# Kernel optimization log

Hardware: AMD Instinct MI355X
Metric: run time of the kernel (lower is better)

## Reference

```python
import jax, jax.numpy as jnp
import numpy as np

BS, DIM = 8192, 768
TEMPERATURE = 1.0
EPS = 1e-8


def setup_inputs() -> dict:
    key = jax.random.key(0)
    k1, k2 = jax.random.split(key)
    text_emb = jax.random.normal(k1, (BS, DIM), dtype=jnp.float32)
    ctr_emb = jax.random.normal(k2, (BS, DIM), dtype=jnp.float32)
    return {"text_emb": text_emb, "ctr_emb": ctr_emb}


def _l2norm(x):
    # cosine scorer normalization
    return x / jnp.maximum(jnp.linalg.norm(x, axis=-1, keepdims=True), EPS)


def reference(text_emb, ctr_emb):
    t = _l2norm(text_emb)          # [bs, d]
    c = _l2norm(ctr_emb)           # [bs, d]
    # S[i, j] = cos(text_i, ctr_j) / T  -- single GEMM instead of (bs,bs,d) broadcast
    S = jnp.einsum('id,jd->ij', t, c) / TEMPERATURE   # [bs, bs]
    sim_ii = jnp.diagonal(S)                           # [bs]
    # loss1_i = lse_j S[i,j] - S[i,i]; loss2_i = lse_j S[j,i] - S[i,i]
    loss = (jax.nn.logsumexp(S, axis=1)
            + jax.nn.logsumexp(S, axis=0)
            - 2.0 * sim_ii)
    return jnp.mean(loss)
```

## Files before the change

kernel.cpp:

```cpp
#include <hip/hip_runtime.h>
#include <hip/hip_bf16.h>

#define BS   8192
#define DIM  768
#define BM   256
#define BK   128
#define NBLK ((BS / BM) * (BS / BM))

typedef float f32x4 __attribute__((ext_vector_type(4)));
typedef int   i32x4 __attribute__((ext_vector_type(4)));
typedef int   i32x8 __attribute__((ext_vector_type(8)));

__device__ __forceinline__ void async16(const void* g, void* l) {
    __builtin_amdgcn_global_load_lds(
        (const __attribute__((address_space(1))) unsigned int*)g,
        (__attribute__((address_space(3))) unsigned int*)l,
        16, 0, 0);
}

__global__ __launch_bounds__(256) void normalize_kernel(
    const float* __restrict__ text, const float* __restrict__ ctr,
    unsigned char* __restrict__ tq, unsigned char* __restrict__ cq,
    float* __restrict__ sim, float* __restrict__ rowsum, float* __restrict__ colsum,
    unsigned int* __restrict__ cnt) {
    if (blockIdx.x < 64) {
        const int i = blockIdx.x * 256 + threadIdx.x;
        rowsum[i] = 0.f;
        colsum[i] = 0.f;
    }
    if (blockIdx.x == 0 && threadIdx.x == 0) cnt[0] = 0u;
    const int lane = threadIdx.x & 63;
    const int row  = blockIdx.x * 4 + (threadIdx.x >> 6);
    const size_t base = (size_t)row * DIM;

    float4 t[3], c[3];
    float st = 0.f, sc = 0.f, sd = 0.f;
#pragma unroll
    for (int i = 0; i < 3; ++i) {
        t[i] = *(const float4*)&text[base + lane * 4 + i * 256];
        c[i] = *(const float4*)&ctr [base + lane * 4 + i * 256];
        st += t[i].x*t[i].x + t[i].y*t[i].y + t[i].z*t[i].z + t[i].w*t[i].w;
        sc += c[i].x*c[i].x + c[i].y*c[i].y + c[i].z*c[i].z + c[i].w*c[i].w;
        sd += t[i].x*c[i].x + t[i].y*c[i].y + t[i].z*c[i].z + t[i].w*c[i].w;
    }
#pragma unroll
    for (int off = 1; off < 64; off <<= 1) {
        st += __shfl_xor(st, off);
        sc += __shfl_xor(sc, off);
        sd += __shfl_xor(sd, off);
    }
    const float invt = 1.0f / fmaxf(sqrtf(st), 1e-8f);
    const float invc = 1.0f / fmaxf(sqrtf(sc), 1e-8f);
#pragma unroll
    for (int i = 0; i < 3; ++i) {
        unsigned int wt = (unsigned int)__builtin_amdgcn_cvt_pk_fp8_f32(t[i].x * invt, t[i].y * invt, 0, false);
        wt = (unsigned int)__builtin_amdgcn_cvt_pk_fp8_f32(t[i].z * invt, t[i].w * invt, (int)wt, true);
        unsigned int wcq = (unsigned int)__builtin_amdgcn_cvt_pk_fp8_f32(c[i].x * invc, c[i].y * invc, 0, false);
        wcq = (unsigned int)__builtin_amdgcn_cvt_pk_fp8_f32(c[i].z * invc, c[i].w * invc, (int)wcq, true);
        *(unsigned int*)&tq[base + lane * 4 + i * 256] = wt;
        *(unsigned int*)&cq[base + lane * 4 + i * 256] = wcq;
    }
    if (lane == 0) sim[row] = sd * invt * invc;
}

__global__ __launch_bounds__(512, 2) void gemm_lse_kernel(
    const unsigned char* __restrict__ tq, const unsigned char* __restrict__ cq,
    float* __restrict__ rowsum, float* __restrict__ colsum,
    const float* __restrict__ sim, unsigned int* __restrict__ cnt,
    float* __restrict__ out) {
    __shared__ char ldsA[2][BM * BK];
    __shared__ char ldsB[2][BM * BK];

    const int tid = threadIdx.x;

    const int bid = blockIdx.x;
    const int xcd = bid & 7, idx = bid >> 3;
    const int tileCol = idx >> 2, rowInBand = idx & 3;
    const int rowBase = (xcd * 4 + rowInBand) * BM;
    const int colBase = tileCol * BM;

    const int wave = tid >> 6, lane = tid & 63;
    const int wr = wave >> 2, wc = wave & 3;
    const int quad = lane >> 4, l16 = lane & 15;

    int goff[4], p16[4];
#pragma unroll
    for (int i = 0; i < 4; ++i) {
        const int p  = tid + i * 512;
        const int kc = p >> 9;
        const int row = (p >> 1) & 255;
        const int hl  = (p & 1) ^ (kc & 1);
        goff[i] = row * DIM + kc * 32 + hl * 16;
        p16[i]  = p * 16;
    }
    const unsigned char* gA = tq + (size_t)rowBase * DIM;
    const unsigned char* gB = cq + (size_t)colBase * DIM;

#define STAGE(buf, t, i)                                            \
    do {                                                            \
        async16(gA + goff[i] + (t) * BK, &ldsA[buf][p16[i]]);       \
        async16(gB + goff[i] + (t) * BK, &ldsB[buf][p16[i]]);       \
    } while (0)

    const int sw = quad & 1;
    int aoff[8], boff[4];
#pragma unroll
    for (int mt = 0; mt < 8; ++mt) aoff[mt] = quad * 8192 + (wr * 128 + mt * 16 + l16) * 32;
#pragma unroll
    for (int nt = 0; nt < 4; ++nt) boff[nt] = quad * 8192 + (wc * 64 + nt * 16 + l16) * 32;

#define RD_A(dst, mt, buf)                                                     \
    do {                                                                       \
        i32x4 lo = *(const i32x4*)(ldsA[buf] + aoff[mt] + sw * 16);            \
        i32x4 hi = *(const i32x4*)(ldsA[buf] + aoff[mt] + (sw ^ 1) * 16);      \
        dst = __builtin_shufflevector(lo, hi, 0, 1, 2, 3, 4, 5, 6, 7);         \
    } while (0)
#define RD_B(dst, nt, buf)                                                     \
    do {                                                                       \
        i32x4 lo = *(const i32x4*)(ldsB[buf] + boff[nt] + sw * 16);            \
        i32x4 hi = *(const i32x4*)(ldsB[buf] + boff[nt] + (sw ^ 1) * 16);      \
        dst = __builtin_shufflevector(lo, hi, 0, 1, 2, 3, 4, 5, 6, 7);         \
    } while (0)
#define MFMA8(a0, a1, m0, m1)                                                  \
    do {                                                                       \
        acc[m0][0] = __builtin_amdgcn_mfma_scale_f32_16x16x128_f8f6f4(a0, bf0, acc[m0][0], 0, 0, 0, 127, 0, 127); \
        acc[m0][1] = __builtin_amdgcn_mfma_scale_f32_16x16x128_f8f6f4(a0, bf1, acc[m0][1], 0, 0, 0, 127, 0, 127); \
        acc[m0][2] = __builtin_amdgcn_mfma_scale_f32_16x16x128_f8f6f4(a0, bf2, acc[m0][2], 0, 0, 0, 127, 0, 127); \
        acc[m0][3] = __builtin_amdgcn_mfma_scale_f32_16x16x128_f8f6f4(a0, bf3, acc[m0][3], 0, 0, 0, 127, 0, 127); \
        acc[m1][0] = __builtin_amdgcn_mfma_scale_f32_16x16x128_f8f6f4(a1, bf0, acc[m1][0], 0, 0, 0, 127, 0, 127); \
        acc[m1][1] = __builtin_amdgcn_mfma_scale_f32_16x16x128_f8f6f4(a1, bf1, acc[m1][1], 0, 0, 0, 127, 0, 127); \
        acc[m1][2] = __builtin_amdgcn_mfma_scale_f32_16x16x128_f8f6f4(a1, bf2, acc[m1][2], 0, 0, 0, 127, 0, 127); \
        acc[m1][3] = __builtin_amdgcn_mfma_scale_f32_16x16x128_f8f6f4(a1, bf3, acc[m1][3], 0, 0, 0, 127, 0, 127); \
    } while (0)
#define SBAR()  __builtin_amdgcn_sched_barrier(0)

    f32x4 acc[8][4];
#pragma unroll
    for (int mt = 0; mt < 8; ++mt)
#pragma unroll
        for (int nt = 0; nt < 4; ++nt)
            acc[mt][nt] = (f32x4){0.f, 0.f, 0.f, 0.f};

    STAGE(0, 0, 0); STAGE(0, 0, 1); STAGE(0, 0, 2); STAGE(0, 0, 3);
    SBAR();
    STAGE(1, 1, 0);
    SBAR();
    asm volatile("s_waitcnt vmcnt(2)" ::: "memory");
    SBAR();
    __builtin_amdgcn_s_barrier();

#pragma unroll
    for (int t = 0; t < 6; ++t) {
        const int cur = t & 1;
        i32x8 bf0, bf1, bf2, bf3, aE0, aE1, aO0, aO1;

        RD_B(bf0, 0, cur); RD_B(bf1, 1, cur); RD_B(bf2, 2, cur); RD_B(bf3, 3, cur);
        RD_A(aE0, 0, cur); RD_A(aE1, 1, cur);

        RD_A(aO0, 2, cur); RD_A(aO1, 3, cur);
        if (t < 5) STAGE(cur ^ 1, t + 1, 1);
        __builtin_amdgcn_s_barrier();
        asm volatile("s_waitcnt lgkmcnt(4)" ::: "memory");
        SBAR();
        __builtin_amdgcn_s_setprio(1);
        MFMA8(aE0, aE1, 0, 1);
        __builtin_amdgcn_s_setprio(0);
        __builtin_amdgcn_s_barrier();

        RD_A(aE0, 4, cur); RD_A(aE1, 5, cur);
        if (t < 5) STAGE(cur ^ 1, t + 1, 2);
        __builtin_amdgcn_s_barrier();
        asm volatile("s_waitcnt lgkmcnt(4)" ::: "memory");
        SBAR();
        __builtin_amdgcn_s_setprio(1);
        MFMA8(aO0, aO1, 2, 3);
        __builtin_amdgcn_s_setprio(0);
        __builtin_amdgcn_s_barrier();

        RD_A(aO0, 6, cur); RD_A(aO1, 7, cur);
        if (t < 5) STAGE(cur ^ 1, t + 1, 3);
        __builtin_amdgcn_s_barrier();
        asm volatile("s_waitcnt lgkmcnt(4)" ::: "memory");
        SBAR();
        __builtin_amdgcn_s_setprio(1);
        MFMA8(aE0, aE1, 4, 5);
        __builtin_amdgcn_s_setprio(0);
        __builtin_amdgcn_s_barrier();

        asm volatile("s_waitcnt lgkmcnt(0)" ::: "memory");
        SBAR();
        if (t < 5) {
            __builtin_amdgcn_s_barrier();
            if (t < 4) STAGE(cur, t + 2, 0);
        }
        __builtin_amdgcn_s_setprio(1);
        MFMA8(aO0, aO1, 6, 7);
        __builtin_amdgcn_s_setprio(0);
        if (t < 5) {
            if (t < 4) asm volatile("s_waitcnt vmcnt(2)" ::: "memory");
            else       asm volatile("s_waitcnt vmcnt(0)" ::: "memory");
            SBAR();
            __builtin_amdgcn_s_barrier();
        }
    }

    float rp[8][4];
    float cp[4];
#pragma unroll
    for (int mt = 0; mt < 8; ++mt)
#pragma unroll
        for (int r = 0; r < 4; ++r) rp[mt][r] = 0.f;
#pragma unroll
    for (int nt = 0; nt < 4; ++nt) cp[nt] = 0.f;

#pragma unroll
    for (int mt = 0; mt < 8; ++mt)
#pragma unroll
        for (int nt = 0; nt < 4; ++nt)
#pragma unroll
            for (int r = 0; r < 4; ++r) {
                const float e = __expf(acc[mt][nt][r]);
                rp[mt][r] += e;
                cp[nt]    += e;
            }

#pragma unroll
    for (int mt = 0; mt < 8; ++mt)
#pragma unroll
        for (int r = 0; r < 4; ++r) {
            float v = rp[mt][r];
            v += __shfl_xor(v, 1);
            v += __shfl_xor(v, 2);
            v += __shfl_xor(v, 4);
            v += __shfl_xor(v, 8);
            rp[mt][r] = v;
        }
    if (l16 == 0) {
#pragma unroll
        for (int mt = 0; mt < 8; ++mt)
#pragma unroll
            for (int r = 0; r < 4; ++r)
                atomicAdd(&rowsum[rowBase + wr * 128 + mt * 16 + quad * 4 + r], rp[mt][r]);
    }
#pragma unroll
    for (int nt = 0; nt < 4; ++nt) {
        float v = cp[nt];
        v += __shfl_xor(v, 16);
        v += __shfl_xor(v, 32);
        if (quad == 0)
            atomicAdd(&colsum[colBase + wc * 64 + nt * 16 + l16], v);
    }

    unsigned int* tick = (unsigned int*)&ldsA[0][0];
    __syncthreads();
    if (tid == 0) {
        __threadfence();
        tick[0] = __hip_atomic_fetch_add(cnt, 1u, __ATOMIC_ACQ_REL, __HIP_MEMORY_SCOPE_AGENT);
    }
    __syncthreads();
    if (tick[0] == NBLK - 1) {
        float a2 = 0.f;
#pragma unroll
        for (int k = 0; k < 16; ++k) {
            const int i = tid + k * 512;
            const float rs = __hip_atomic_load(&rowsum[i], __ATOMIC_RELAXED, __HIP_MEMORY_SCOPE_AGENT);
            const float cs = __hip_atomic_load(&colsum[i], __ATOMIC_RELAXED, __HIP_MEMORY_SCOPE_AGENT);
            a2 += __logf(rs) + __logf(cs) - 2.f * sim[i];
        }
#pragma unroll
        for (int off = 1; off < 64; off <<= 1) a2 += __shfl_xor(a2, off);
        float* red = (float*)&ldsB[0][0];
        if (lane == 0) red[wave] = a2;
        __syncthreads();
        if (tid == 0) {
            float s = 0.f;
#pragma unroll
            for (int w = 0; w < 8; ++w) s += red[w];
            out[0] = s / (float)BS;
        }
    }
}

extern "C" void kernel_launch(void* const* d_in, const int* in_sizes, int n_in,
                              void* d_out, int out_size, void* d_ws, size_t ws_size,
                              hipStream_t stream) {
    const float* text = (const float*)d_in[0];
    const float* ctr  = (const float*)d_in[1];

    char* ws = (char*)d_ws;
    const size_t embBytes = (size_t)BS * DIM;
    unsigned char* tq = (unsigned char*)ws;
    unsigned char* cq = (unsigned char*)(ws + embBytes);
    float* sim    = (float*)(ws + 2 * embBytes);
    float* rowsum = (float*)(ws + 2 * embBytes + BS * sizeof(float));
    float* colsum = (float*)(ws + 2 * embBytes + 2 * BS * sizeof(float));
    unsigned int* cnt = (unsigned int*)(ws + 2 * embBytes + 3 * BS * sizeof(float));

    normalize_kernel<<<BS / 4, 256, 0, stream>>>(text, ctr, tq, cq, sim, rowsum, colsum, cnt);

    gemm_lse_kernel<<<NBLK, 512, 0, stream>>>(tq, cq, rowsum, colsum, sim, cnt, (float*)d_out);
}
```

Baseline: 200.7 us.

## Fuse normalize and GEMM-LSE into one persistent kernel with grid barrier

Merges the normalize/quantize kernel and the GEMM+logsumexp kernel into a single persistent launch of 256 blocks. The blocks first normalize rows, then meet at a global atomic grid barrier, and each block then processes 4 column tiles in a loop. The extra per-stage s_barriers inside the K loop are also dropped. This removes one kernel launch and the tail of the second grid, but it relies on all 256 blocks being co-resident, adds a memset launch, and gives up some latency hiding from the removed barriers.

```diff
diff --git a/kernel.cpp b/kernel.cpp
--- a/kernel.cpp
+++ b/kernel.cpp
@@ -1,11 +1,11 @@
 #include <hip/hip_runtime.h>
 #include <hip/hip_bf16.h>
 
-#define BS   8192
-#define DIM  768
-#define BM   256
-#define BK   128
-#define NBLK ((BS / BM) * (BS / BM))
+#define BS    8192
+#define DIM   768
+#define BM    256
+#define BK    128
+#define NPERS 256
 
 typedef float f32x4 __attribute__((ext_vector_type(4)));
 typedef int   i32x4 __attribute__((ext_vector_type(4)));
@@ -18,70 +18,72 @@
         16, 0, 0);
 }
 
-__global__ __launch_bounds__(256) void normalize_kernel(
+__global__ __launch_bounds__(512, 2) void fused_kernel(
     const float* __restrict__ text, const float* __restrict__ ctr,
     unsigned char* __restrict__ tq, unsigned char* __restrict__ cq,
     float* __restrict__ sim, float* __restrict__ rowsum, float* __restrict__ colsum,
-    unsigned int* __restrict__ cnt) {
-    if (blockIdx.x < 64) {
-        const int i = blockIdx.x * 256 + threadIdx.x;
+    unsigned int* __restrict__ syncv, float* __restrict__ out) {
+    __shared__ char ldsA[2][BM * BK];
+    __shared__ char ldsB[2][BM * BK];
+
+    const int tid  = threadIdx.x;
+    const int bid  = blockIdx.x;
+    const int wave = tid >> 6, lane = tid & 63;
+
+    if (bid < 32) {
+        const int i = bid * 512 + tid;
         rowsum[i] = 0.f;
         colsum[i] = 0.f;
     }
-    if (blockIdx.x == 0 && threadIdx.x == 0) cnt[0] = 0u;
-    const int lane = threadIdx.x & 63;
-    const int row  = blockIdx.x * 4 + (threadIdx.x >> 6);
-    const size_t base = (size_t)row * DIM;
-
-    float4 t[3], c[3];
-    float st = 0.f, sc = 0.f, sd = 0.f;
-#pragma unroll
-    for (int i = 0; i < 3; ++i) {
-        t[i] = *(const float4*)&text[base + lane * 4 + i * 256];
-        c[i] = *(const float4*)&ctr [base + lane * 4 + i * 256];
-        st += t[i].x*t[i].x + t[i].y*t[i].y + t[i].z*t[i].z + t[i].w*t[i].w;
-        sc += c[i].x*c[i].x + c[i].y*c[i].y + c[i].z*c[i].z + c[i].w*c[i].w;
-        sd += t[i].x*c[i].x + t[i].y*c[i].y + t[i].z*c[i].z + t[i].w*c[i].w;
-    }
-#pragma unroll
-    for (int off = 1; off < 64; off <<= 1) {
-        st += __shfl_xor(st, off);
-        sc += __shfl_xor(sc, off);
-        sd += __shfl_xor(sd, off);
-    }
-    const float invt = 1.0f / fmaxf(sqrtf(st), 1e-8f);
-    const float invc = 1.0f / fmaxf(sqrtf(sc), 1e-8f);
-#pragma unroll
-    for (int i = 0; i < 3; ++i) {
-        unsigned int wt = (unsigned int)__builtin_amdgcn_cvt_pk_fp8_f32(t[i].x * invt, t[i].y * invt, 0, false);
-        wt = (unsigned int)__builtin_amdgcn_cvt_pk_fp8_f32(t[i].z * invt, t[i].w * invt, (int)wt, true);
-        unsigned int wcq = (unsigned int)__builtin_amdgcn_cvt_pk_fp8_f32(c[i].x * invc, c[i].y * invc, 0, false);
-        wcq = (unsigned int)__builtin_amdgcn_cvt_pk_fp8_f32(c[i].z * invc, c[i].w * invc, (int)wcq, true);
-        *(unsigned int*)&tq[base + lane * 4 + i * 256] = wt;
-        *(unsigned int*)&cq[base + lane * 4 + i * 256] = wcq;
-    }
-    if (lane == 0) sim[row] = sd * invt * invc;
-}
-
-__global__ __launch_bounds__(512, 2) void gemm_lse_kernel(
-    const unsigned char* __restrict__ tq, const unsigned char* __restrict__ cq,
-    float* __restrict__ rowsum, float* __restrict__ colsum,
-    const float* __restrict__ sim, unsigned int* __restrict__ cnt,
-    float* __restrict__ out) {
-    __shared__ char ldsA[2][BM * BK];
-    __shared__ char ldsB[2][BM * BK];
-
-    const int tid = threadIdx.x;
-
-    const int bid = blockIdx.x;
-    const int xcd = bid & 7, idx = bid >> 3;
-    const int tileCol = idx >> 2, rowInBand = idx & 3;
-    const int rowBase = (xcd * 4 + rowInBand) * BM;
-    const int colBase = tileCol * BM;
-
-    const int wave = tid >> 6, lane = tid & 63;
+#pragma unroll
+    for (int r = 0; r < 4; ++r) {
+        const int row = bid * 32 + wave * 4 + r;
+        const size_t base = (size_t)row * DIM;
+        float4 t[3], c[3];
+        float st = 0.f, sc = 0.f, sd = 0.f;
+#pragma unroll
+        for (int i = 0; i < 3; ++i) {
+            t[i] = *(const float4*)&text[base + lane * 4 + i * 256];
+            c[i] = *(const float4*)&ctr [base + lane * 4 + i * 256];
+            st += t[i].x*t[i].x + t[i].y*t[i].y + t[i].z*t[i].z + t[i].w*t[i].w;
+            sc += c[i].x*c[i].x + c[i].y*c[i].y + c[i].z*c[i].z + c[i].w*c[i].w;
+            sd += t[i].x*c[i].x + t[i].y*c[i].y + t[i].z*c[i].z + t[i].w*c[i].w;
+        }
+#pragma unroll
+        for (int off = 1; off < 64; off <<= 1) {
+            st += __shfl_xor(st, off);
+            sc += __shfl_xor(sc, off);
+            sd += __shfl_xor(sd, off);
+        }
+        const float invt = 1.0f / fmaxf(sqrtf(st), 1e-8f);
+        const float invc = 1.0f / fmaxf(sqrtf(sc), 1e-8f);
+#pragma unroll
+        for (int i = 0; i < 3; ++i) {
+            unsigned int wt = (unsigned int)__builtin_amdgcn_cvt_pk_fp8_f32(t[i].x * invt, t[i].y * invt, 0, false);
+            wt = (unsigned int)__builtin_amdgcn_cvt_pk_fp8_f32(t[i].z * invt, t[i].w * invt, (int)wt, true);
+            unsigned int wcq = (unsigned int)__builtin_amdgcn_cvt_pk_fp8_f32(c[i].x * invc, c[i].y * invc, 0, false);
+            wcq = (unsigned int)__builtin_amdgcn_cvt_pk_fp8_f32(c[i].z * invc, c[i].w * invc, (int)wcq, true);
+            *(unsigned int*)&tq[base + lane * 4 + i * 256] = wt;
+            *(unsigned int*)&cq[base + lane * 4 + i * 256] = wcq;
+        }
+        if (lane == 0) sim[row] = sd * invt * invc;
+    }
+
+    __syncthreads();
+    if (tid == 0) {
+        __threadfence();
+        __hip_atomic_fetch_add(&syncv[0], 1u, __ATOMIC_ACQ_REL, __HIP_MEMORY_SCOPE_AGENT);
+        while (__hip_atomic_load(&syncv[0], __ATOMIC_RELAXED, __HIP_MEMORY_SCOPE_AGENT) < NPERS)
+            __builtin_amdgcn_s_sleep(1);
+        __threadfence();
+    }
+    __syncthreads();
+
     const int wr = wave >> 2, wc = wave & 3;
     const int quad = lane >> 4, l16 = lane & 15;
+
+    const int rowBase = ((bid & 7) * 4 + ((bid >> 3) & 3)) * BM;
+    const unsigned char* gA = tq + (size_t)rowBase * DIM;
 
     int goff[4], p16[4];
 #pragma unroll
@@ -93,22 +95,19 @@
         goff[i] = row * DIM + kc * 32 + hl * 16;
         p16[i]  = p * 16;
     }
-    const unsigned char* gA = tq + (size_t)rowBase * DIM;
-    const unsigned char* gB = cq + (size_t)colBase * DIM;
+
+    const int sw = quad & 1;
+    int aoff[8], boff[4];
+#pragma unroll
+    for (int mt = 0; mt < 8; ++mt) aoff[mt] = quad * 8192 + (wr * 128 + mt * 16 + l16) * 32;
+#pragma unroll
+    for (int nt = 0; nt < 4; ++nt) boff[nt] = quad * 8192 + (wc * 64 + nt * 16 + l16) * 32;
 
 #define STAGE(buf, t, i)                                            \
     do {                                                            \
         async16(gA + goff[i] + (t) * BK, &ldsA[buf][p16[i]]);       \
         async16(gB + goff[i] + (t) * BK, &ldsB[buf][p16[i]]);       \
     } while (0)
-
-    const int sw = quad & 1;
-    int aoff[8], boff[4];
-#pragma unroll
-    for (int mt = 0; mt < 8; ++mt) aoff[mt] = quad * 8192 + (wr * 128 + mt * 16 + l16) * 32;
-#pragma unroll
-    for (int nt = 0; nt < 4; ++nt) boff[nt] = quad * 8192 + (wc * 64 + nt * 16 + l16) * 32;
-
 #define RD_A(dst, mt, buf)                                                     \
     do {                                                                       \
         i32x4 lo = *(const i32x4*)(ldsA[buf] + aoff[mt] + sw * 16);            \
@@ -134,131 +133,137 @@
     } while (0)
 #define SBAR()  __builtin_amdgcn_sched_barrier(0)
 
-    f32x4 acc[8][4];
-#pragma unroll
-    for (int mt = 0; mt < 8; ++mt)
-#pragma unroll
-        for (int nt = 0; nt < 4; ++nt)
-            acc[mt][nt] = (f32x4){0.f, 0.f, 0.f, 0.f};
-
-    STAGE(0, 0, 0); STAGE(0, 0, 1); STAGE(0, 0, 2); STAGE(0, 0, 3);
-    SBAR();
-    STAGE(1, 1, 0);
-    SBAR();
-    asm volatile("s_waitcnt vmcnt(2)" ::: "memory");
-    SBAR();
-    __builtin_amdgcn_s_barrier();
-
-#pragma unroll
-    for (int t = 0; t < 6; ++t) {
-        const int cur = t & 1;
-        i32x8 bf0, bf1, bf2, bf3, aE0, aE1, aO0, aO1;
-
-        RD_B(bf0, 0, cur); RD_B(bf1, 1, cur); RD_B(bf2, 2, cur); RD_B(bf3, 3, cur);
-        RD_A(aE0, 0, cur); RD_A(aE1, 1, cur);
-
-        RD_A(aO0, 2, cur); RD_A(aO1, 3, cur);
-        if (t < 5) STAGE(cur ^ 1, t + 1, 1);
+#pragma unroll 1
+    for (int rep = 0; rep < 4; ++rep) {
+        const int colBase = (rep * 8 + (bid >> 5)) * BM;
+        const unsigned char* gB = cq + (size_t)colBase * DIM;
+
+        f32x4 acc[8][4];
+#pragma unroll
+        for (int mt = 0; mt < 8; ++mt)
+#pragma unroll
+            for (int nt = 0; nt < 4; ++nt)
+                acc[mt][nt] = (f32x4){0.f, 0.f, 0.f, 0.f};
+
+        __syncthreads();
+
+        STAGE(0, 0, 0); STAGE(0, 0, 1); STAGE(0, 0, 2); STAGE(0, 0, 3);
+        SBAR();
+        STAGE(1, 1, 0);
+        SBAR();
+        asm volatile("s_waitcnt vmcnt(2)" ::: "memory");
+        SBAR();
         __builtin_amdgcn_s_barrier();
-        asm volatile("s_waitcnt lgkmcnt(4)" ::: "memory");
-        SBAR();
-        __builtin_amdgcn_s_setprio(1);
-        MFMA8(aE0, aE1, 0, 1);
-        __builtin_amdgcn_s_setprio(0);
-        __builtin_amdgcn_s_barrier();
-
-        RD_A(aE0, 4, cur); RD_A(aE1, 5, cur);
-        if (t < 5) STAGE(cur ^ 1, t + 1, 2);
-        __builtin_amdgcn_s_barrier();
-        asm volatile("s_waitcnt lgkmcnt(4)" ::: "memory");
-        SBAR();
-        __builtin_amdgcn_s_setprio(1);
-        MFMA8(aO0, aO1, 2, 3);
-        __builtin_amdgcn_s_setprio(0);
-        __builtin_amdgcn_s_barrier();
-
-        RD_A(aO0, 6, cur); RD_A(aO1, 7, cur);
-        if (t < 5) STAGE(cur ^ 1, t + 1, 3);
-        __builtin_amdgcn_s_barrier();
-        asm volatile("s_waitcnt lgkmcnt(4)" ::: "memory");
-        SBAR();
-        __builtin_amdgcn_s_setprio(1);
-        MFMA8(aE0, aE1, 4, 5);
-        __builtin_amdgcn_s_setprio(0);
-        __builtin_amdgcn_s_barrier();
-
-        asm volatile("s_waitcnt lgkmcnt(0)" ::: "memory");
-        SBAR();
-        if (t < 5) {
-            __builtin_amdgcn_s_barrier();
-            if (t < 4) STAGE(cur, t + 2, 0);
-        }
-        __builtin_amdgcn_s_setprio(1);
-        MFMA8(aO0, aO1, 6, 7);
-        __builtin_amdgcn_s_setprio(0);
-        if (t < 5) {
-            if (t < 4) asm volatile("s_waitcnt vmcnt(2)" ::: "memory");
-            else       asm volatile("s_waitcnt vmcnt(0)" ::: "memory");
+
+#pragma unroll
+        for (int t = 0; t < 6; ++t) {
+            const int cur = t & 1;
+            i32x8 bf0, bf1, bf2, bf3, aE0, aE1, aO0, aO1;
+
+            RD_B(bf0, 0, cur); RD_B(bf1, 1, cur); RD_B(bf2, 2, cur); RD_B(bf3, 3, cur);
+            RD_A(aE0, 0, cur); RD_A(aE1, 1, cur);
+
+            RD_A(aO0, 2, cur); RD_A(aO1, 3, cur);
+            if (t < 5) STAGE(cur ^ 1, t + 1, 1);
+            asm volatile("s_waitcnt lgkmcnt(4)" ::: "memory");
             SBAR();
-            __builtin_amdgcn_s_barrier();
-        }
-    }
-
-    float rp[8][4];
-    float cp[4];
-#pragma unroll
-    for (int mt = 0; mt < 8; ++mt)
-#pragma unroll
-        for (int r = 0; r < 4; ++r) rp[mt][r] = 0.f;
-#pragma unroll
-    for (int nt = 0; nt < 4; ++nt) cp[nt] = 0.f;
-
-#pragma unroll
-    for (int mt = 0; mt < 8; ++mt)
-#pragma unroll
-        for (int nt = 0; nt < 4; ++nt)
+            __builtin_amdgcn_s_setprio(1);
+            MFMA8(aE0, aE1, 0, 1);
+            __builtin_amdgcn_s_setprio(0);
+
+            RD_A(aE0, 4, cur); RD_A(aE1, 5, cur);
+            if (t < 5) STAGE(cur ^ 1, t + 1, 2);
+            asm volatile("s_waitcnt lgkmcnt(4)" ::: "memory");
+            SBAR();
+            __builtin_amdgcn_s_setprio(1);
+            MFMA8(aO0, aO1, 2, 3);
+            __builtin_amdgcn_s_setprio(0);
+
+            RD_A(aO0, 6, cur); RD_A(aO1, 7, cur);
+            if (t < 5) STAGE(cur ^ 1, t + 1, 3);
+            asm volatile("s_waitcnt lgkmcnt(4)" ::: "memory");
+            SBAR();
+            __builtin_amdgcn_s_setprio(1);
+            MFMA8(aE0, aE1, 4, 5);
+            __builtin_amdgcn_s_setprio(0);
+
+            asm volatile("s_waitcnt lgkmcnt(0)" ::: "memory");
+            SBAR();
+            __builtin_amdgcn_s_setprio(1);
+            MFMA8(aO0, aO1, 6, 7);
+            __builtin_amdgcn_s_setprio(0);
+
+            if (t < 5) {
+                __builtin_amdgcn_s_barrier();
+                SBAR();
+                if (t < 4) {
+                    STAGE(cur, t + 2, 0);
+                    SBAR();
+                    asm volatile("s_waitcnt vmcnt(2)" ::: "memory");
+                } else {
+                    asm volatile("s_waitcnt vmcnt(0)" ::: "memory");
+                }
+                SBAR();
+                __builtin_amdgcn_s_barrier();
+            }
+        }
+
+        float rp[8][4];
+        float cp[4];
+#pragma unroll
+        for (int mt = 0; mt < 8; ++mt)
+#pragma unroll
+            for (int r = 0; r < 4; ++r) rp[mt][r] = 0.f;
+#pragma unroll
+        for (int nt = 0; nt < 4; ++nt) cp[nt] = 0.f;
+
+#pragma unroll
+        for (int mt = 0; mt < 8; ++mt)
+#pragma unroll
+            for (int nt = 0; nt < 4; ++nt)
+#pragma unroll
+                for (int r = 0; r < 4; ++r) {
+                    const float e = __expf(acc[mt][nt][r]);
+                    rp[mt][r] += e;
+                    cp[nt]    += e;
+                }
+
+#pragma unroll
+        for (int mt = 0; mt < 8; ++mt)
 #pragma unroll
             for (int r = 0; r < 4; ++r) {
-                const float e = __expf(acc[mt][nt][r]);
-                rp[mt][r] += e;
-                cp[nt]    += e;
+                float v = rp[mt][r];
+                v += __shfl_xor(v, 1);
+                v += __shfl_xor(v, 2);
+                v += __shfl_xor(v, 4);
+                v += __shfl_xor(v, 8);
+                rp[mt][r] = v;
             }
-
-#pragma unroll
-    for (int mt = 0; mt < 8; ++mt)
-#pragma unroll
-        for (int r = 0; r < 4; ++r) {
-            float v = rp[mt][r];
-            v += __shfl_xor(v, 1);
-            v += __shfl_xor(v, 2);
-            v += __shfl_xor(v, 4);
-            v += __shfl_xor(v, 8);
-            rp[mt][r] = v;
-        }
-    if (l16 == 0) {
-#pragma unroll
-        for (int mt = 0; mt < 8; ++mt)
-#pragma unroll
-            for (int r = 0; r < 4; ++r)
-                atomicAdd(&rowsum[rowBase + wr * 128 + mt * 16 + quad * 4 + r], rp[mt][r]);
-    }
-#pragma unroll
-    for (int nt = 0; nt < 4; ++nt) {
-        float v = cp[nt];
-        v += __shfl_xor(v, 16);
-        v += __shfl_xor(v, 32);
-        if (quad == 0)
-            atomicAdd(&colsum[colBase + wc * 64 + nt * 16 + l16], v);
+        if (l16 == 0) {
+#pragma unroll
+            for (int mt = 0; mt < 8; ++mt)
+#pragma unroll
+                for (int r = 0; r < 4; ++r)
+                    atomicAdd(&rowsum[rowBase + wr * 128 + mt * 16 + quad * 4 + r], rp[mt][r]);
+        }
+#pragma unroll
+        for (int nt = 0; nt < 4; ++nt) {
+            float v = cp[nt];
+            v += __shfl_xor(v, 16);
+            v += __shfl_xor(v, 32);
+            if (quad == 0)
+                atomicAdd(&colsum[colBase + wc * 64 + nt * 16 + l16], v);
+        }
     }
 
     unsigned int* tick = (unsigned int*)&ldsA[0][0];
     __syncthreads();
     if (tid == 0) {
         __threadfence();
-        tick[0] = __hip_atomic_fetch_add(cnt, 1u, __ATOMIC_ACQ_REL, __HIP_MEMORY_SCOPE_AGENT);
+        tick[0] = __hip_atomic_fetch_add(&syncv[1], 1u, __ATOMIC_ACQ_REL, __HIP_MEMORY_SCOPE_AGENT);
     }
     __syncthreads();
-    if (tick[0] == NBLK - 1) {
+    if (tick[0] == NPERS - 1) {
         float a2 = 0.f;
 #pragma unroll
         for (int k = 0; k < 16; ++k) {
@@ -294,9 +299,10 @@
     float* sim    = (float*)(ws + 2 * embBytes);
     float* rowsum = (float*)(ws + 2 * embBytes + BS * sizeof(float));
     float* colsum = (float*)(ws + 2 * embBytes + 2 * BS * sizeof(float));
-    unsigned int* cnt = (unsigned int*)(ws + 2 * embBytes + 3 * BS * sizeof(float));
-
-    normalize_kernel<<<BS / 4, 256, 0, stream>>>(text, ctr, tq, cq, sim, rowsum, colsum, cnt);
-
-    gemm_lse_kernel<<<NBLK, 512, 0, stream>>>(tq, cq, rowsum, colsum, sim, cnt, (float*)d_out);
+    unsigned int* syncv = (unsigned int*)(ws + 2 * embBytes + 3 * BS * sizeof(float));
+
+    hipMemsetAsync(syncv, 0, 8, stream);
+
+    fused_kernel<<<NPERS, 512, 0, stream>>>(text, ctr, tq, cq, sim,
+                                            rowsum, colsum, syncv, (float*)d_out);
 }
```

After: 240.0 us. 19.6% more time.
